# Kernel tuning notes

Measured on AMD Instinct MI355X. Metric: run time of the kernel, lower is better.

The kernel has to match this reference:

```python
import jax, jax.numpy as jnp
import numpy as np

LAGRANGE_ORDER = 5  # fixed, as in the torch module


def _lagrange_weights(alpha):
    """Vectorised Lagrange weights of length L+1. alpha: [B,N] -> [B,N,L+1]."""
    L = LAGRANGE_ORDER
    j = jnp.arange(L + 1, dtype=alpha.dtype)
    u = alpha[..., None] - j                          # [B,N,L+1]
    denom = j[:, None] - j[None, :]                   # [L+1,L+1]
    mask = ~jnp.eye(L + 1, dtype=bool)
    num = jnp.where(mask, u[..., None, :], jnp.ones_like(u)[..., None, :])
    den = jnp.where(mask, denom, jnp.ones_like(denom))
    return (num / den).prod(axis=-1)                  # [B,N,L+1]


def setup_inputs() -> dict:
    key = jax.random.key(0)
    k1, k2, k3 = jax.random.split(key, 3)
    B, N = 16, 16384
    # fractional period in samples, in [40, 100) -> max floor(f0)=99, K=99+5+3=107<=108
    f0 = 40.0 + 60.0 * jax.random.uniform(k1, (B, N), dtype=jnp.float32)
    x = jax.random.normal(k2, (B, N), dtype=jnp.float32)
    l_b = jax.random.uniform(k3, (B, N, 2), dtype=jnp.float32)  # (g, p) in [0,1]
    return {"f0": f0, "x": x, "l_b": l_b, "K": 108}


def reference(f0, x, l_b, K):
    B, N = x.shape
    L = LAGRANGE_ORDER
    # design_loop: (g, p) -> loop taps [b0, a1]; gain capped <1 for stability
    g = 0.99 * l_b[..., 0]
    p = l_b[..., 1]
    b0 = g * (1.0 - p)                                # [B,N]
    a1 = g * p
    # tune_f0: subtract low-frequency phase delay of (b0 + a1 z^-1)
    f0c = f0 - a1 / (b0 + a1 + 1e-7)
    # Lagrange centre & weights
    z = jnp.floor(f0c).astype(jnp.int32)
    z_center = z - L // 2                             # [B,N]
    alpha = f0c - z_center.astype(f0.dtype)
    w = _lagrange_weights(alpha)                      # [B,N,L+1]
    # compute_resonator_matrix: loop filter convolved with fractional delay -> block [B,N,L+2]
    block = (b0[..., None] * jnp.pad(w, ((0, 0), (0, 0), (0, 1)))
             + a1[..., None] * jnp.pad(w, ((0, 0), (0, 0), (1, 0))))
    # scatter (-block) into A; LPC lag k+1 lives in column k
    cols = z_center[..., None] - 1 + jnp.arange(L + 2)  # [B,N,L+2]
    cols = jnp.clip(cols, 0, K - 1)
    A = jnp.zeros((B, N, K), x.dtype).at[
        jnp.arange(B)[:, None, None], jnp.arange(N)[None, :, None], cols
    ].add(-block)
    # sample_wise_lpc: y[n] = x[n] - sum_k A[n,k] * y[n-1-k], zero init state
    def step(buf, inp):
        a_n, x_n = inp                                 # [B,K], [B]
        y_n = x_n - jnp.sum(a_n * buf, axis=-1)
        buf = jnp.concatenate([y_n[:, None], buf[:, :-1]], axis=1)
        return buf, y_n
    buf0 = jnp.zeros((B, K), x.dtype)
    _, ys = jax.lax.scan(step, buf0, (A.transpose(1, 0, 2), x.T))  # ys: [N,B]
    return ys.T
```

## Files before the change

### kernel.cpp

```cpp
#include <hip/hip_runtime.h>
#include <math.h>


#define B_    16
#define N_    16384
#define S_    16
#define NSEG  1024
#define NITER 28
#define RUNS  104
#define CHUNK 37

#define TG_FLOATS (B_ * S_ * RUNS * RUNS)
#define ST_FLOATS (B_ * S_ * RUNS)

__device__ __forceinline__ void diffks_coeffs(float f0v, float lbg, float lbp,
                                              int n, float4& lo, float4& hi) {
  float g  = 0.99f * lbg;
  float p  = lbp;
  float b0 = g * (1.0f - p);
  float a1 = g * p;
  float f0c = f0v - a1 / (b0 + a1 + 1e-7f);
  int   zc  = (int)floorf(f0c) - 2;
  float alpha = f0c - (float)zc;
  float u0 = alpha;
  float u1 = alpha - 1.0f;
  float u2 = alpha - 2.0f;
  float u3 = alpha - 3.0f;
  float u4 = alpha - 4.0f;
  float u5 = alpha - 5.0f;
  float w0 = u1 * u2 * u3 * u4 * u5 * (-1.0f / 120.0f);
  float w1 = u0 * u2 * u3 * u4 * u5 * ( 1.0f /  24.0f);
  float w2 = u0 * u1 * u3 * u4 * u5 * (-1.0f /  12.0f);
  float w3 = u0 * u1 * u2 * u4 * u5 * ( 1.0f /  12.0f);
  float w4 = u0 * u1 * u2 * u3 * u5 * (-1.0f /  24.0f);
  float w5 = u0 * u1 * u2 * u3 * u4 * ( 1.0f / 120.0f);
  lo.x = b0 * w0;
  lo.y = fmaf(b0, w1, a1 * w0);
  lo.z = fmaf(b0, w2, a1 * w1);
  lo.w = fmaf(b0, w3, a1 * w2);
  hi.x = fmaf(b0, w4, a1 * w3);
  hi.y = fmaf(b0, w5, a1 * w4);
  hi.z = a1 * w5;
  hi.w = __int_as_float((n - 6 - zc) & 255);
}

__global__ __launch_bounds__(1024) void diffks_phase1(
    const float* __restrict__ f0, const float* __restrict__ lb,
    const float* __restrict__ x, float* __restrict__ Tg) {
  const int bs = blockIdx.x;
  const int b  = bs >> 4, s = bs & 15;
  const int n0 = s << 10;
  const int tid = threadIdx.x;

  __shared__ __align__(16) float hist[256 * RUNS];
  __shared__ float4 sLo[NSEG], sHi[NSEG];
  __shared__ float  sX[NSEG];

  {
    const size_t gi = (size_t)b * N_ + n0 + tid;
    float4 lo, hi;
    diffks_coeffs(f0[gi], lb[2 * gi], lb[2 * gi + 1], tid, lo, hi);
    sLo[tid] = lo; sHi[tid] = hi; sX[tid] = x[gi];
  }
  for (int i = tid; i < 64 * RUNS; i += 1024)
    ((float4*)hist)[i] = float4{0.0f, 0.0f, 0.0f, 0.0f};
  __syncthreads();
  if (tid < 103) hist[(255 - tid) * RUNS + tid] = 1.0f;
  __syncthreads();

  const int w    = tid >> 6;
  const int lane = tid & 63;
  const int cl   = 2 * lane;
  const bool act = (lane < 52);
  const bool px  = (lane == 51);

  for (int t = 0; t < 32; ++t) {
#pragma unroll
    for (int u = 0; u < 2; ++u) {
      const int p = 32 * t + 2 * w + u;
      const float4 lo = sLo[p];
      const float4 hi = sHi[p];
      const float  xv = sX[p];
      if (act) {
        const int base = __float_as_int(hi.w);
        float2 acc;
        acc.x = 0.0f;
        acc.y = px ? xv : 0.0f;
        const float c[7] = {hi.z, hi.y, hi.x, lo.w, lo.z, lo.y, lo.x};
#pragma unroll
        for (int m = 0; m < 7; ++m) {
          const int row = (base + m) & 255;
          const float2 v = *(const float2*)&hist[row * RUNS + cl];
          acc.x = fmaf(c[m], v.x, acc.x);
          acc.y = fmaf(c[m], v.y, acc.y);
        }
        *(float2*)&hist[(p & 255) * RUNS + cl] = acc;
      }
    }
    __syncthreads();
  }

  float* __restrict__ T = Tg + (size_t)bs * RUNS * RUNS;
  for (int idx = tid; idx < RUNS * RUNS; idx += 1024) {
    const int r = idx / RUNS;
    const int j = idx - r * RUNS;
    T[idx] = (j < 103) ? hist[((255 - j) & 255) * RUNS + r] : 0.0f;
  }
}

__global__ __launch_bounds__(832) void diffks_phase2(
    const float* __restrict__ Tg, float* __restrict__ states) {
  const int b   = blockIdx.x;
  const int tid = threadIdx.x;
  const int j   = tid % RUNS;
  const int q   = tid / RUNS;
  const int r0  = 13 * q;
  __shared__ float cur[RUNS];
  __shared__ float part[8][105];
  if (tid < 103) cur[tid] = 0.0f;
  if (tid == 103) cur[103] = 1.0f;
  __syncthreads();

  const float* __restrict__ Tb = Tg + (size_t)b * S_ * RUNS * RUNS;
  float tvA[13], tvB[13];
#pragma unroll
  for (int k = 0; k < 13; ++k) {
    tvA[k] = Tb[(size_t)(r0 + k) * RUNS + j];
    tvB[k] = Tb[(size_t)RUNS * RUNS + (size_t)(r0 + k) * RUNS + j];
  }

#pragma unroll
  for (int s = 0; s < S_; ++s) {
    float* tv = (s & 1) ? tvB : tvA;
    if (q == 0) states[((size_t)b * S_ + s) * RUNS + j] = cur[j];
    float acc = 0.0f;
#pragma unroll
    for (int k = 0; k < 13; ++k) acc = fmaf(tv[k], cur[r0 + k], acc);
    if (s + 2 < S_) {
      const float* __restrict__ Tn = Tb + (size_t)(s + 2) * RUNS * RUNS;
#pragma unroll
      for (int k = 0; k < 13; ++k)
        tv[k] = Tn[(size_t)(r0 + k) * RUNS + j];
    }
    part[q][j] = acc;
    __syncthreads();
    if (q == 0) {
      float v = 0.0f;
#pragma unroll
      for (int qq = 0; qq < 8; ++qq) v += part[qq][j];
      cur[j] = (j < 103) ? v : 1.0f;
    }
    __syncthreads();
  }
}

__global__ __launch_bounds__(256) void diffks_phase3(
    const float* __restrict__ f0, const float* __restrict__ lb,
    const float* __restrict__ x, const float* __restrict__ states,
    float* __restrict__ y) {
  const int bs = blockIdx.x;
  const int b  = bs >> 4, s = bs & 15;
  const int n0 = s << 10;
  const int tid = threadIdx.x;

  __shared__ __align__(16) float ring[512];
  __shared__ float4 sC[2 * NSEG];
  __shared__ float  sX[NSEG];
  __shared__ float  sY[NSEG];

  for (int i = tid; i < 512; i += 256) ring[i] = 0.0f;
  for (int i = tid; i < NSEG; i += 256) {
    const int n = n0 + i;
    const size_t gi = (size_t)b * N_ + n;
    float4 lo, hi;
    diffks_coeffs(f0[gi], lb[2 * gi], lb[2 * gi + 1], n, lo, hi);
    sC[2 * i] = lo; sC[2 * i + 1] = hi; sX[i] = x[gi];
  }
  __syncthreads();
  const float* __restrict__ st = states + (size_t)bs * RUNS;
  for (int k = tid; k < 103; k += 256) {
    const float v = st[k];
    ring[255 - k] = v;
    ring[511 - k] = v;
  }
  __syncthreads();

  if (tid < 64) {
    const int lane = tid;
    const bool act = (lane < CHUNK);
    for (int t = 0; t < NITER; ++t) {
      const int p = t * CHUNK + lane;
      if (act && p < NSEG) {
        const float4 lo = sC[2 * p];
        const float4 hi = sC[2 * p + 1];
        const float  xv = sX[p];
        const int base = __float_as_int(hi.w);
        const float r0 = ring[base + 0];
        const float r1 = ring[base + 1];
        const float r2 = ring[base + 2];
        const float r3 = ring[base + 3];
        const float r4 = ring[base + 4];
        const float r5 = ring[base + 5];
        const float r6 = ring[base + 6];
        const float s0 = fmaf(lo.x, r6, xv);
        const float s1 = fmaf(lo.y, r5, lo.z * r4);
        const float s2 = fmaf(lo.w, r3, hi.x * r2);
        const float s3 = fmaf(hi.y, r1, hi.z * r0);
        const float yv = (s0 + s1) + (s2 + s3);
        const int wsl = p & 255;
        ring[wsl]       = yv;
        ring[wsl + 256] = yv;
        sY[p] = yv;
      }
      __builtin_amdgcn_wave_barrier();
      asm volatile("" ::: "memory");
    }
  }
  __syncthreads();

  float4* __restrict__ yb = (float4*)(y + (size_t)b * N_ + n0);
  yb[tid] = ((const float4*)sY)[tid];
}

__global__ __launch_bounds__(256) void diffks_coeff_fb(
    const float* __restrict__ f0, const float* __restrict__ lb,
    float* __restrict__ cw, int total, int Nmask) {
  int idx = blockIdx.x * blockDim.x + threadIdx.x;
  if (idx >= total) return;
  float4 lo, hi;
  diffks_coeffs(f0[idx], lb[2 * idx], lb[2 * idx + 1], idx & Nmask, lo, hi);
  float4* out4 = (float4*)cw;
  out4[2 * idx]     = lo;
  out4[2 * idx + 1] = hi;
}

__global__ __launch_bounds__(64) void diffks_scan_fb(
    const float* __restrict__ x, const float* __restrict__ cw,
    float* __restrict__ y, int N) {
  const int b    = blockIdx.x;
  const int lane = threadIdx.x;
  __shared__ float ring[512];
#pragma unroll
  for (int i = 0; i < 8; ++i) ring[lane + 64 * i] = 0.0f;
  __builtin_amdgcn_wave_barrier();
  asm volatile("" ::: "memory");
  const float4* __restrict__ c4 = (const float4*)(cw + (size_t)b * N * 8);
  const float*  __restrict__ xb = x + (size_t)b * N;
  float*        __restrict__ yb = y + (size_t)b * N;
  const bool act = (lane < CHUNK);
  const int nIter = (N + CHUNK - 1) / CHUNK;
  for (int t = 0; t < nIter; ++t) {
    const int n = t * CHUNK + lane;
    if (act && n < N) {
      const float4 lo = c4[2 * n];
      const float4 hi = c4[2 * n + 1];
      const float  xv = xb[n];
      const int base = __float_as_int(hi.w);
      const float r0 = ring[base + 0];
      const float r1 = ring[base + 1];
      const float r2 = ring[base + 2];
      const float r3 = ring[base + 3];
      const float r4 = ring[base + 4];
      const float r5 = ring[base + 5];
      const float r6 = ring[base + 6];
      const float s0 = fmaf(lo.x, r6, xv);
      const float s1 = fmaf(lo.y, r5, lo.z * r4);
      const float s2 = fmaf(lo.w, r3, hi.x * r2);
      const float s3 = fmaf(hi.y, r1, hi.z * r0);
      const float yv = (s0 + s1) + (s2 + s3);
      ring[n & 255]         = yv;
      ring[(n & 255) + 256] = yv;
      yb[n] = yv;
    }
    __builtin_amdgcn_wave_barrier();
    asm volatile("" ::: "memory");
  }
}

extern "C" void kernel_launch(void* const* d_in, const int* in_sizes, int n_in,
                              void* d_out, int out_size, void* d_ws, size_t ws_size,
                              hipStream_t stream) {
  const float* f0 = (const float*)d_in[0];
  const float* x  = (const float*)d_in[1];
  const float* lb = (const float*)d_in[2];
  float* out = (float*)d_out;

  const int total = in_sizes[0];
  const size_t need = (size_t)(TG_FLOATS + ST_FLOATS) * 4;

  if (total == B_ * N_ && ws_size >= need) {
    float* Tg = (float*)d_ws;
    float* st = Tg + TG_FLOATS;
    diffks_phase1<<<B_ * S_, 1024, 0, stream>>>(f0, lb, x, Tg);
    diffks_phase2<<<B_, 832, 0, stream>>>(Tg, st);
    diffks_phase3<<<B_ * S_, 256, 0, stream>>>(f0, lb, x, st, out);
  } else {
    const int N = total / B_;
    float* cw = (float*)d_ws;
    diffks_coeff_fb<<<(total + 255) / 256, 256, 0, stream>>>(f0, lb, cw, total, N - 1);
    diffks_scan_fb<<<B_, 64, 0, stream>>>(x, cw, out, N);
  }
}
```

Measured before the change: 105.8 us.

## Fuse state-propagation and segment scan kernels into one per-batch block

Merges phase2 (cross-segment state propagation) and phase3 (per-segment scan) into one kernel with 1024 threads per batch. The 16 segment states stay in shared memory, and each of the 16 waves then runs one segment's sequential scan with its own ring buffer. Coefficients are computed inline from register-prefetched inputs and outputs are written straight to global memory. This removes one launch and the global round-trip of states, but the final scans now run on only 16 blocks instead of 256, so they are serialised behind phase2 per batch with less parallelism and less coefficient precompute overlap.

```diff
diff --git a/kernel.cpp b/kernel.cpp
--- a/kernel.cpp
+++ b/kernel.cpp
@@ -108,15 +108,22 @@
   }
 }
 
-__global__ __launch_bounds__(832) void diffks_phase2(
-    const float* __restrict__ Tg, float* __restrict__ states) {
+__global__ __launch_bounds__(1024) void diffks_phase23(
+    const float* __restrict__ Tg, const float* __restrict__ f0,
+    const float* __restrict__ lb, const float* __restrict__ x,
+    float* __restrict__ y) {
   const int b   = blockIdx.x;
   const int tid = threadIdx.x;
   const int j   = tid % RUNS;
   const int q   = tid / RUNS;
+  const bool a2 = (q < 8);
   const int r0  = 13 * q;
+
+  __shared__ float stAll[S_ * RUNS];
   __shared__ float cur[RUNS];
   __shared__ float part[8][105];
+  __shared__ __align__(16) float ring[16 * 512];
+
   if (tid < 103) cur[tid] = 0.0f;
   if (tid == 103) cur[103] = 1.0f;
   __syncthreads();
@@ -125,14 +132,14 @@
   float tvA[13], tvB[13];
 #pragma unroll
   for (int k = 0; k < 13; ++k) {
-    tvA[k] = Tb[(size_t)(r0 + k) * RUNS + j];
-    tvB[k] = Tb[(size_t)RUNS * RUNS + (size_t)(r0 + k) * RUNS + j];
+    tvA[k] = a2 ? Tb[(size_t)(r0 + k) * RUNS + j] : 0.0f;
+    tvB[k] = a2 ? Tb[(size_t)RUNS * RUNS + (size_t)(r0 + k) * RUNS + j] : 0.0f;
   }
 
 #pragma unroll
   for (int s = 0; s < S_; ++s) {
     float* tv = (s & 1) ? tvB : tvA;
-    if (q == 0) states[((size_t)b * S_ + s) * RUNS + j] = cur[j];
+    if (q == 0) stAll[s * RUNS + j] = cur[j];
     float acc = 0.0f;
 #pragma unroll
     for (int k = 0; k < 13; ++k) acc = fmaf(tv[k], cur[r0 + k], acc);
@@ -140,9 +147,9 @@
       const float* __restrict__ Tn = Tb + (size_t)(s + 2) * RUNS * RUNS;
 #pragma unroll
       for (int k = 0; k < 13; ++k)
-        tv[k] = Tn[(size_t)(r0 + k) * RUNS + j];
-    }
-    part[q][j] = acc;
+        tv[k] = a2 ? Tn[(size_t)(r0 + k) * RUNS + j] : 0.0f;
+    }
+    if (a2) part[q][j] = acc;
     __syncthreads();
     if (q == 0) {
       float v = 0.0f;
@@ -152,74 +159,78 @@
     }
     __syncthreads();
   }
-}
-
-__global__ __launch_bounds__(256) void diffks_phase3(
-    const float* __restrict__ f0, const float* __restrict__ lb,
-    const float* __restrict__ x, const float* __restrict__ states,
-    float* __restrict__ y) {
-  const int bs = blockIdx.x;
-  const int b  = bs >> 4, s = bs & 15;
-  const int n0 = s << 10;
-  const int tid = threadIdx.x;
-
-  __shared__ __align__(16) float ring[512];
-  __shared__ float4 sC[2 * NSEG];
-  __shared__ float  sX[NSEG];
-  __shared__ float  sY[NSEG];
-
-  for (int i = tid; i < 512; i += 256) ring[i] = 0.0f;
-  for (int i = tid; i < NSEG; i += 256) {
-    const int n = n0 + i;
-    const size_t gi = (size_t)b * N_ + n;
-    float4 lo, hi;
-    diffks_coeffs(f0[gi], lb[2 * gi], lb[2 * gi + 1], n, lo, hi);
-    sC[2 * i] = lo; sC[2 * i + 1] = hi; sX[i] = x[gi];
-  }
-  __syncthreads();
-  const float* __restrict__ st = states + (size_t)bs * RUNS;
-  for (int k = tid; k < 103; k += 256) {
-    const float v = st[k];
-    ring[255 - k] = v;
-    ring[511 - k] = v;
-  }
-  __syncthreads();
-
-  if (tid < 64) {
-    const int lane = tid;
-    const bool act = (lane < CHUNK);
-    for (int t = 0; t < NITER; ++t) {
-      const int p = t * CHUNK + lane;
-      if (act && p < NSEG) {
-        const float4 lo = sC[2 * p];
-        const float4 hi = sC[2 * p + 1];
-        const float  xv = sX[p];
-        const int base = __float_as_int(hi.w);
-        const float r0 = ring[base + 0];
-        const float r1 = ring[base + 1];
-        const float r2 = ring[base + 2];
-        const float r3 = ring[base + 3];
-        const float r4 = ring[base + 4];
-        const float r5 = ring[base + 5];
-        const float r6 = ring[base + 6];
-        const float s0 = fmaf(lo.x, r6, xv);
-        const float s1 = fmaf(lo.y, r5, lo.z * r4);
-        const float s2 = fmaf(lo.w, r3, hi.x * r2);
-        const float s3 = fmaf(hi.y, r1, hi.z * r0);
-        const float yv = (s0 + s1) + (s2 + s3);
-        const int wsl = p & 255;
-        ring[wsl]       = yv;
-        ring[wsl + 256] = yv;
-        sY[p] = yv;
+
+  const int w    = tid >> 6;
+  const int lane = tid & 63;
+  float* __restrict__ R = ring + (w << 9);
+
+#pragma unroll
+  for (int i = 0; i < 8; ++i) R[lane + 64 * i] = 0.0f;
+  __builtin_amdgcn_wave_barrier();
+  asm volatile("" ::: "memory");
+  {
+    if (lane < 103) {
+      const float v = stAll[w * RUNS + lane];
+      R[255 - lane] = v; R[511 - lane] = v;
+    }
+    if (lane < 39) {
+      const float v = stAll[w * RUNS + lane + 64];
+      R[191 - lane] = v; R[447 - lane] = v;
+    }
+  }
+  __builtin_amdgcn_wave_barrier();
+  asm volatile("" ::: "memory");
+
+  const int n0 = w << 10;
+  const size_t gb = (size_t)b * N_ + n0;
+  const float*  __restrict__ f0b = f0 + gb;
+  const float2* __restrict__ lbb = (const float2*)(lb + 2 * gb);
+  const float*  __restrict__ xb  = x + gb;
+  float*        __restrict__ yb  = y + gb;
+  const bool al = (lane < CHUNK);
+
+  float  rf[2]; float2 rl[2]; float rx[2];
+  if (al) {
+    rf[0] = f0b[lane];          rl[0] = lbb[lane];          rx[0] = xb[lane];
+    rf[1] = f0b[lane + CHUNK];  rl[1] = lbb[lane + CHUNK];  rx[1] = xb[lane + CHUNK];
+  }
+
+  for (int t = 0; t < NITER; ++t) {
+    const int p = t * CHUNK + lane;
+    const int st = t & 1;
+    const float  cf = rf[st];
+    const float2 cl2 = rl[st];
+    const float  cx = rx[st];
+    {
+      const int p2 = p + 2 * CHUNK;
+      if (al && p2 < NSEG) {
+        rf[st] = f0b[p2]; rl[st] = lbb[p2]; rx[st] = xb[p2];
       }
-      __builtin_amdgcn_wave_barrier();
-      asm volatile("" ::: "memory");
-    }
-  }
-  __syncthreads();
-
-  float4* __restrict__ yb = (float4*)(y + (size_t)b * N_ + n0);
-  yb[tid] = ((const float4*)sY)[tid];
+    }
+    if (al && p < NSEG) {
+      float4 lo, hi;
+      diffks_coeffs(cf, cl2.x, cl2.y, p, lo, hi);
+      const int base = __float_as_int(hi.w);
+      const float t0 = R[base + 0];
+      const float t1 = R[base + 1];
+      const float t2 = R[base + 2];
+      const float t3 = R[base + 3];
+      const float t4 = R[base + 4];
+      const float t5 = R[base + 5];
+      const float t6 = R[base + 6];
+      const float s0 = fmaf(lo.x, t6, cx);
+      const float s1 = fmaf(lo.y, t5, lo.z * t4);
+      const float s2 = fmaf(lo.w, t3, hi.x * t2);
+      const float s3 = fmaf(hi.y, t1, hi.z * t0);
+      const float yv = (s0 + s1) + (s2 + s3);
+      const int wsl = p & 255;
+      R[wsl]       = yv;
+      R[wsl + 256] = yv;
+      yb[p] = yv;
+    }
+    __builtin_amdgcn_wave_barrier();
+    asm volatile("" ::: "memory");
+  }
 }
 
 __global__ __launch_bounds__(256) void diffks_coeff_fb(
@@ -290,10 +301,8 @@
 
   if (total == B_ * N_ && ws_size >= need) {
     float* Tg = (float*)d_ws;
-    float* st = Tg + TG_FLOATS;
     diffks_phase1<<<B_ * S_, 1024, 0, stream>>>(f0, lb, x, Tg);
-    diffks_phase2<<<B_, 832, 0, stream>>>(Tg, st);
-    diffks_phase3<<<B_ * S_, 256, 0, stream>>>(f0, lb, x, st, out);
+    diffks_phase23<<<B_, 1024, 0, stream>>>(Tg, f0, lb, x, out);
   } else {
     const int N = total / B_;
     float* cw = (float*)d_ws;
```

Result: slower. 122.8 us (+16.1%).

## Fuse segment-state composition into scan kernel, dropping the separate phase2 launch

Applied to the files above, without the earlier changes.

Removes the sequential phase2 kernel that composed the per-segment transfer matrices for each batch. Each scan block now recomputes its own starting state by composing the transfer matrices of all earlier segments in one wave, using double-buffered float2 register loads. The other three waves compute coefficients in parallel with that work. This saves a kernel launch and the global round trip of the states, but later segments repeat up to 15 matrix-vector products serially, so the last segments carry more latency than before.

```diff
diff --git a/kernel.cpp b/kernel.cpp
--- a/kernel.cpp
+++ b/kernel.cpp
@@ -11,7 +11,6 @@
 #define CHUNK 37
 
 #define TG_FLOATS (B_ * S_ * RUNS * RUNS)
-#define ST_FLOATS (B_ * S_ * RUNS)
 
 __device__ __forceinline__ void diffks_coeffs(float f0v, float lbg, float lbp,
                                               int n, float4& lo, float4& hi) {
@@ -108,55 +107,20 @@
   }
 }
 
-__global__ __launch_bounds__(832) void diffks_phase2(
-    const float* __restrict__ Tg, float* __restrict__ states) {
-  const int b   = blockIdx.x;
-  const int tid = threadIdx.x;
-  const int j   = tid % RUNS;
-  const int q   = tid / RUNS;
-  const int r0  = 13 * q;
-  __shared__ float cur[RUNS];
-  __shared__ float part[8][105];
-  if (tid < 103) cur[tid] = 0.0f;
-  if (tid == 103) cur[103] = 1.0f;
-  __syncthreads();
-
-  const float* __restrict__ Tb = Tg + (size_t)b * S_ * RUNS * RUNS;
-  float tvA[13], tvB[13];
-#pragma unroll
-  for (int k = 0; k < 13; ++k) {
-    tvA[k] = Tb[(size_t)(r0 + k) * RUNS + j];
-    tvB[k] = Tb[(size_t)RUNS * RUNS + (size_t)(r0 + k) * RUNS + j];
-  }
-
-#pragma unroll
-  for (int s = 0; s < S_; ++s) {
-    float* tv = (s & 1) ? tvB : tvA;
-    if (q == 0) states[((size_t)b * S_ + s) * RUNS + j] = cur[j];
-    float acc = 0.0f;
-#pragma unroll
-    for (int k = 0; k < 13; ++k) acc = fmaf(tv[k], cur[r0 + k], acc);
-    if (s + 2 < S_) {
-      const float* __restrict__ Tn = Tb + (size_t)(s + 2) * RUNS * RUNS;
-#pragma unroll
-      for (int k = 0; k < 13; ++k)
-        tv[k] = Tn[(size_t)(r0 + k) * RUNS + j];
-    }
-    part[q][j] = acc;
-    __syncthreads();
-    if (q == 0) {
-      float v = 0.0f;
-#pragma unroll
-      for (int qq = 0; qq < 8; ++qq) v += part[qq][j];
-      cur[j] = (j < 103) ? v : 1.0f;
-    }
-    __syncthreads();
-  }
-}
-
-__global__ __launch_bounds__(256) void diffks_phase3(
-    const float* __restrict__ f0, const float* __restrict__ lb,
-    const float* __restrict__ x, const float* __restrict__ states,
+
+#define CG_LOAD(BUF, Tbase, rbase)                                           \
+  { _Pragma("unroll") for (int kk = 0; kk < 13; ++kk)                        \
+      BUF[kk] = *(const float2*)&(Tbase)[((rbase) + kk) * RUNS + cl]; }
+
+#define CG_FMA(BUF, rbase)                                                   \
+  { _Pragma("unroll") for (int kk = 0; kk < 13; ++kk) {                      \
+      const float cv = curL[(rbase) + kk];                                   \
+      acc[kk & 3].x = fmaf(BUF[kk].x, cv, acc[kk & 3].x);                    \
+      acc[kk & 3].y = fmaf(BUF[kk].y, cv, acc[kk & 3].y); } }
+
+__global__ __launch_bounds__(256, 1) void diffks_compose_scan(
+    const float* __restrict__ Tg, const float* __restrict__ f0,
+    const float* __restrict__ lb, const float* __restrict__ x,
     float* __restrict__ y) {
   const int bs = blockIdx.x;
   const int b  = bs >> 4, s = bs & 15;
@@ -164,24 +128,70 @@
   const int tid = threadIdx.x;
 
   __shared__ __align__(16) float ring[512];
-  __shared__ float4 sC[2 * NSEG];
+  __shared__ __align__(16) float4 sC[2 * NSEG];
   __shared__ float  sX[NSEG];
   __shared__ float  sY[NSEG];
-
-  for (int i = tid; i < 512; i += 256) ring[i] = 0.0f;
-  for (int i = tid; i < NSEG; i += 256) {
-    const int n = n0 + i;
-    const size_t gi = (size_t)b * N_ + n;
-    float4 lo, hi;
-    diffks_coeffs(f0[gi], lb[2 * gi], lb[2 * gi + 1], n, lo, hi);
-    sC[2 * i] = lo; sC[2 * i + 1] = hi; sX[i] = x[gi];
-  }
-  __syncthreads();
-  const float* __restrict__ st = states + (size_t)bs * RUNS;
-  for (int k = tid; k < 103; k += 256) {
-    const float v = st[k];
-    ring[255 - k] = v;
-    ring[511 - k] = v;
+  __shared__ float  curL[RUNS];
+
+  ring[tid] = 0.0f; ring[tid + 256] = 0.0f;
+  if (tid < 52) {
+    float2 iv; iv.x = 0.0f; iv.y = (tid == 51) ? 1.0f : 0.0f;
+    *(float2*)&curL[2 * tid] = iv;
+  }
+  __syncthreads();
+
+  if (tid < 64) {
+    const int l  = tid;
+    const int cl = 2 * l;
+    if (l < 52 && s > 0) {
+      const float* __restrict__ Tb = Tg + (size_t)(b * S_) * RUNS * RUNS;
+      float2 B0[13], B1[13], B2[13], B3[13];
+      float2 acc[4];
+      CG_LOAD(B0, Tb, 0)
+      CG_LOAD(B1, Tb, 13)
+      CG_LOAD(B2, Tb, 26)
+      CG_LOAD(B3, Tb, 39)
+      for (int k = 0; k < s; ++k) {
+        const float* __restrict__ Tk = Tb + (size_t)k * RUNS * RUNS;
+        const float* __restrict__ Tn =
+            Tb + (size_t)((k + 1 < s) ? k + 1 : k) * RUNS * RUNS;
+#pragma unroll
+        for (int a = 0; a < 4; ++a) { acc[a].x = 0.0f; acc[a].y = 0.0f; }
+        CG_FMA(B0, 0)   CG_LOAD(B0, Tk, 52)
+        CG_FMA(B1, 13)  CG_LOAD(B1, Tk, 65)
+        CG_FMA(B2, 26)  CG_LOAD(B2, Tk, 78)
+        CG_FMA(B3, 39)  CG_LOAD(B3, Tk, 91)
+        CG_FMA(B0, 52)  CG_LOAD(B0, Tn, 0)
+        CG_FMA(B1, 65)  CG_LOAD(B1, Tn, 13)
+        CG_FMA(B2, 78)  CG_LOAD(B2, Tn, 26)
+        CG_FMA(B3, 91)  CG_LOAD(B3, Tn, 39)
+        float2 nw;
+        nw.x = (acc[0].x + acc[1].x) + (acc[2].x + acc[3].x);
+        nw.y = (acc[0].y + acc[1].y) + (acc[2].y + acc[3].y);
+        if (l == 51) nw.y = 1.0f;
+        *(float2*)&curL[cl] = nw;
+        __builtin_amdgcn_wave_barrier();
+        asm volatile("" ::: "memory");
+      }
+    }
+    __builtin_amdgcn_wave_barrier();
+    asm volatile("" ::: "memory");
+    {
+      const float v = curL[l];
+      ring[255 - l] = v; ring[511 - l] = v;
+      if (l < 39) {
+        const float v2 = curL[l + 64];
+        ring[191 - l] = v2; ring[447 - l] = v2;
+      }
+    }
+  } else {
+    const size_t gb = (size_t)b * N_ + n0;
+    for (int i = tid - 64; i < NSEG; i += 192) {
+      const size_t gi = gb + i;
+      float4 lo, hi;
+      diffks_coeffs(f0[gi], lb[2 * gi], lb[2 * gi + 1], n0 + i, lo, hi);
+      sC[2 * i] = lo; sC[2 * i + 1] = hi; sX[i] = x[gi];
+    }
   }
   __syncthreads();
 
@@ -286,14 +296,12 @@
   float* out = (float*)d_out;
 
   const int total = in_sizes[0];
-  const size_t need = (size_t)(TG_FLOATS + ST_FLOATS) * 4;
+  const size_t need = (size_t)TG_FLOATS * 4;
 
   if (total == B_ * N_ && ws_size >= need) {
     float* Tg = (float*)d_ws;
-    float* st = Tg + TG_FLOATS;
     diffks_phase1<<<B_ * S_, 1024, 0, stream>>>(f0, lb, x, Tg);
-    diffks_phase2<<<B_, 832, 0, stream>>>(Tg, st);
-    diffks_phase3<<<B_ * S_, 256, 0, stream>>>(f0, lb, x, st, out);
+    diffks_compose_scan<<<B_ * S_, 256, 0, stream>>>(Tg, f0, lb, x, out);
   } else {
     const int N = total / B_;
     float* cw = (float*)d_ws;
```

Measured after the change: 112.9 us. 6.7% more time.
